# Kernel tuning notes

Measured on AMD Instinct MI355X. Metric: run time of the kernel, lower is better.

## Reference

```python
import jax, jax.numpy as jnp
import numpy as np

B, S, D, H = 2, 2048, 1024, 16
DH = D // H
LEVELS, FACTOR = 3, 2


def setup_inputs() -> dict:
    key = jax.random.key(0)
    ks = jax.random.split(key, 12)
    s = 1.0 / np.sqrt(D)
    n = lambda k, shape, sc: (jax.random.normal(k, shape, jnp.float32) * sc)
    return {
        "query": n(ks[0], (B, S, D), 1.0),
        "key": n(ks[1], (B, S, D), 1.0),
        "value": n(ks[2], (B, S, D), 1.0),
        "Wq": n(ks[3], (D, D), s), "bq": jnp.zeros((D,), jnp.float32),
        "Wk": n(ks[4], (D, D), s), "bk": jnp.zeros((D,), jnp.float32),
        "Wv": n(ks[5], (D, D), s), "bv": jnp.zeros((D,), jnp.float32),
        "Wo": n(ks[6], (D, D), s), "bo": jnp.zeros((D,), jnp.float32),
        "w_levels": jnp.ones((LEVELS,), jnp.float32),
    }


def _downsample(m):
    # mean-pool pairs along sequence: [B, S, D] -> [B, S//FACTOR, D]
    b, s, d = m.shape
    sn = s // FACTOR
    return m[:, : sn * FACTOR, :].reshape(b, sn, FACTOR, d).mean(axis=2)


def _mha(q, k, v, Wq, bq, Wk, bk, Wv, bv, Wo, bo):
    b, sq, d = q.shape
    sk = k.shape[1]
    qh = (q @ Wq + bq).reshape(b, sq, H, DH)
    kh = (k @ Wk + bk).reshape(b, sk, H, DH)
    vh = (v @ Wv + bv).reshape(b, sk, H, DH)
    scores = jnp.einsum("bqhd,bkhd->bhqk", qh, kh) / np.sqrt(DH)
    attn = jax.nn.softmax(scores, axis=-1)
    out = jnp.einsum("bhqk,bkhd->bqhd", attn, vh).reshape(b, sq, d)
    return out @ Wo + bo


def reference(query, key, value, Wq, bq, Wk, bk, Wv, bv, Wo, bo, w_levels):
    keys, vals = [key], [value]
    k_, v_ = key, value
    for _ in range(LEVELS - 1):
        k_ = _downsample(k_)
        v_ = _downsample(v_)
        keys.append(k_)
        vals.append(v_)
    acc = None
    for lvl in range(LEVELS):
        o = _mha(query, keys[lvl], vals[lvl], Wq, bq, Wk, bk, Wv, bv, Wo, bo)
        o = o * w_levels[lvl]
        acc = o if acc is None else acc + o
    return acc / w_levels.sum()
```

## Files before the change

kernel.cpp:

```cpp
#include <hip/hip_runtime.h>


#define B_  2
#define S_  2048
#define D_  1024
#define H_  16
#define DH_ 64
#define THR2 10.0f

typedef short s8v __attribute__((ext_vector_type(8)));
typedef float f4v __attribute__((ext_vector_type(4)));
typedef float f16v __attribute__((ext_vector_type(16)));
typedef unsigned int u32x2 __attribute__((ext_vector_type(2)));
typedef unsigned int u32x4 __attribute__((ext_vector_type(4)));

__device__ __forceinline__ unsigned cvtpk(float lo, float hi){
    unsigned r;
    asm volatile("v_cvt_pk_bf16_f32 %0, %1, %2" : "=v"(r) : "v"(lo), "v"(hi));
    return r;
}
__device__ __forceinline__ unsigned short f2bf1(float v){
    unsigned r;
    asm volatile("v_cvt_pk_bf16_f32 %0, %1, %2" : "=v"(r) : "v"(v), "v"(v));
    return (unsigned short)r;
}
__device__ __forceinline__ float bf2f(unsigned short h){
    union { unsigned u; float f; } v; v.u = ((unsigned)h) << 16;
    return v.f;
}
__device__ __forceinline__ float exp2_(float x){
    float r; asm("v_exp_f32 %0, %1" : "=v"(r) : "v"(x)); return r;
}
__device__ __forceinline__ void pswap(unsigned &dst, unsigned &src){
    asm volatile("v_permlane32_swap_b32 %0, %1" : "+v"(dst), "+v"(src));
}
__device__ __forceinline__ int swz(int row, int kb){
    return row*128 + (((kb) ^ (row & 7) ^ ((row >> 3) & 7)) << 4);
}

__global__ __launch_bounds__(256) void wtrans(
    const float* __restrict__ W0, const float* __restrict__ W1,
    const float* __restrict__ W2, const float* __restrict__ W3,
    unsigned short* __restrict__ T0, unsigned short* __restrict__ T1,
    unsigned short* __restrict__ T2, unsigned short* __restrict__ T3)
{
    __shared__ float tl[32][33];
    const float* W = blockIdx.z==0?W0: blockIdx.z==1?W1: blockIdx.z==2?W2:W3;
    unsigned short* T = blockIdx.z==0?T0: blockIdx.z==1?T1: blockIdx.z==2?T2:T3;
    const int t = threadIdx.x;
    const int bk = blockIdx.x*32, bn = blockIdx.y*32;
    {
        int row = t>>3, c4 = (t&7)*4;
        float4 v = *(const float4*)&W[(size_t)(bk+row)*D_ + bn + c4];
        tl[row][c4+0]=v.x; tl[row][c4+1]=v.y; tl[row][c4+2]=v.z; tl[row][c4+3]=v.w;
    }
    __syncthreads();
    {
        int n = t>>3, k4 = (t&7)*4;
        unsigned a = cvtpk(tl[k4+0][n], tl[k4+1][n]);
        unsigned b = cvtpk(tl[k4+2][n], tl[k4+3][n]);
        u32x2 pk = {a, b};
        *(u32x2*)&T[(size_t)(bn+n)*D_ + bk + k4] = pk;
    }
}

template<int MODE, int AF32>
__global__ __launch_bounds__(256) void gemm_mfma(
    const void* __restrict__ Av, const unsigned short* __restrict__ Btw,
    const float* __restrict__ bias, void* __restrict__ Cv, float scale)
{
    const int N_ = D_, K_ = D_;
    __shared__ __align__(16) char lds[65536];
    const int t = threadIdx.x;
    const int l = t & 63, wv = t>>6, g = l>>4, x = l&15;
    const int wr = wv>>1, wc = wv&1;
    const int br = blockIdx.y*128, bc = blockIdx.x*128;
    const float* Af = (const float*)Av;
    const unsigned short* Ab = (const unsigned short*)Av;

    int rw[4], bl[4];
    #pragma unroll
    for (int p=0;p<4;++p){ int u = t + 256*p; rw[p] = u>>3; bl[p] = u&7; }

    f4v acc[4][4];
    #pragma unroll
    for (int i=0;i<4;++i)
        #pragma unroll
        for (int j=0;j<4;++j) acc[i][j] = (f4v){0.f,0.f,0.f,0.f};

    float4 alo[4], ahi[4]; s8v arg[4]; s8v brg[4];
    #pragma unroll
    for (int p=0;p<4;++p){
        if (AF32){
            const float* ap = Af + (size_t)(br+rw[p])*K_ + bl[p]*8;
            alo[p] = *(const float4*)ap; ahi[p] = *(const float4*)(ap+4);
        } else {
            arg[p] = *(const s8v*)(Ab + (size_t)(br+rw[p])*K_ + bl[p]*8);
        }
        brg[p] = *(const s8v*)(Btw + (size_t)(bc+rw[p])*K_ + bl[p]*8);
    }

    int cur = 0;
    for (int kt=0; kt<K_; kt+=64){
        char* AsB = lds + cur*32768;
        char* BsB = AsB + 16384;
        #pragma unroll
        for (int p=0;p<4;++p){
            if (AF32){
                uint4 pk;
                pk.x = cvtpk(alo[p].x, alo[p].y); pk.y = cvtpk(alo[p].z, alo[p].w);
                pk.z = cvtpk(ahi[p].x, ahi[p].y); pk.w = cvtpk(ahi[p].z, ahi[p].w);
                *(uint4*)(AsB + swz(rw[p], bl[p])) = pk;
            } else {
                *(s8v*)(AsB + swz(rw[p], bl[p])) = arg[p];
            }
            *(s8v*)(BsB + swz(rw[p], bl[p])) = brg[p];
        }
        if (kt + 64 < K_){
            #pragma unroll
            for (int p=0;p<4;++p){
                if (AF32){
                    const float* ap = Af + (size_t)(br+rw[p])*K_ + (kt+64) + bl[p]*8;
                    alo[p] = *(const float4*)ap; ahi[p] = *(const float4*)(ap+4);
                } else {
                    arg[p] = *(const s8v*)(Ab + (size_t)(br+rw[p])*K_ + (kt+64) + bl[p]*8);
                }
                brg[p] = *(const s8v*)(Btw + (size_t)(bc+rw[p])*K_ + (kt+64) + bl[p]*8);
            }
        }
        __syncthreads();
        #pragma unroll
        for (int c=0;c<2;++c){
            s8v af[4], bf[4];
            #pragma unroll
            for (int fm=0; fm<4; ++fm)
                af[fm] = *(const s8v*)(AsB + swz(wr*64+fm*16+x, c*4+g));
            #pragma unroll
            for (int fn=0; fn<4; ++fn)
                bf[fn] = *(const s8v*)(BsB + swz(wc*64+fn*16+x, c*4+g));
            __builtin_amdgcn_s_setprio(1);
            #pragma unroll
            for (int fm=0; fm<4; ++fm)
                #pragma unroll
                for (int fn=0; fn<4; ++fn)
                    acc[fm][fn] = __builtin_amdgcn_mfma_f32_16x16x32_bf16(
                        af[fm], bf[fn], acc[fm][fn], 0,0,0);
            __builtin_amdgcn_s_setprio(0);
        }
        cur ^= 1;
    }

    #pragma unroll
    for (int fn=0; fn<4; ++fn){
        int col = bc + wc*64 + fn*16 + x;
        float bv = bias[col];
        #pragma unroll
        for (int fm=0; fm<4; ++fm){
            int row0 = br + wr*64 + fm*16 + g*4;
            float v0 = (acc[fm][fn][0] + bv);
            float v1 = (acc[fm][fn][1] + bv);
            float v2 = (acc[fm][fn][2] + bv);
            float v3 = (acc[fm][fn][3] + bv);
            if (MODE == 0){
                float* C = (float*)Cv;
                C[(size_t)(row0+0)*N_ + col] = v0;
                C[(size_t)(row0+1)*N_ + col] = v1;
                C[(size_t)(row0+2)*N_ + col] = v2;
                C[(size_t)(row0+3)*N_ + col] = v3;
            } else if (MODE == 1){
                unsigned short* C = (unsigned short*)Cv;
                int hI = col>>6, dhI = col & (DH_-1);
                #pragma unroll
                for (int r=0;r<4;++r){
                    int row = row0 + r;
                    int bI = row>>11, sI = row & (S_-1);
                    float vv = (r==0?v0: r==1?v1: r==2?v2: v3) * scale;
                    C[(((size_t)(bI*H_+hI))*S_+sI)*DH_+dhI] = f2bf1(vv);
                }
            } else {
                unsigned short* C = (unsigned short*)Cv;
                int bI = row0>>11, sI = row0 & (S_-1);
                int hI = col>>6, dhI = col & (DH_-1);
                u32x2 pk;
                pk.x = cvtpk(v0*scale, v1*scale);
                pk.y = cvtpk(v2*scale, v3*scale);
                *(u32x2*)&C[(((size_t)(bI*H_+hI))*DH_+dhI)*S_ + sI] = pk;
            }
        }
    }
}

__global__ __launch_bounds__(256) void pool2_bf16(
    const unsigned short* __restrict__ in, unsigned short* __restrict__ out,
    int nOut4, int Sin)
{
    int idx = blockIdx.x * 256 + threadIdx.x;
    if (idx >= nOut4) return;
    int d0   = (idx & 15) * 4;
    int rest = idx >> 4;
    int Sout = Sin >> 1;
    int so = rest % Sout;
    int bh = rest / Sout;
    size_t base = ((size_t)bh * Sin + 2*so) * DH_ + d0;
    ushort4 a = *(const ushort4*)&in[base];
    ushort4 c = *(const ushort4*)&in[base + DH_];
    ushort4 o;
    o.x = f2bf1(0.5f*(bf2f(a.x)+bf2f(c.x)));
    o.y = f2bf1(0.5f*(bf2f(a.y)+bf2f(c.y)));
    o.z = f2bf1(0.5f*(bf2f(a.z)+bf2f(c.z)));
    o.w = f2bf1(0.5f*(bf2f(a.w)+bf2f(c.w)));
    *(ushort4*)&out[(size_t)idx*4] = o;
}

__global__ __launch_bounds__(256) void pool2T(
    const unsigned short* __restrict__ in, unsigned short* __restrict__ out,
    int nOut4, int Sin, int shift)
{
    int idx = blockIdx.x * 256 + threadIdx.x;
    if (idx >= nOut4) return;
    int row = idx >> shift;
    int so4 = (idx & ((1<<shift)-1)) << 2;
    union { u32x4 u; unsigned short h[8]; } a;
    a.u = *(const u32x4*)&in[(size_t)row*Sin + so4*2];
    float m0 = 0.5f*(bf2f(a.h[0])+bf2f(a.h[1]));
    float m1 = 0.5f*(bf2f(a.h[2])+bf2f(a.h[3]));
    float m2 = 0.5f*(bf2f(a.h[4])+bf2f(a.h[5]));
    float m3 = 0.5f*(bf2f(a.h[6])+bf2f(a.h[7]));
    u32x2 pk; pk.x = cvtpk(m0,m1); pk.y = cvtpk(m2,m3);
    *(u32x2*)&out[(size_t)row*(Sin>>1) + so4] = pk;
}

__global__ __launch_bounds__(256, 2) void attn_mfma5(
    const unsigned short* __restrict__ qh,
    const unsigned short* __restrict__ kh0, const unsigned short* __restrict__ kh1,
    const unsigned short* __restrict__ kh2,
    const unsigned short* __restrict__ vt0, const unsigned short* __restrict__ vt1,
    const unsigned short* __restrict__ vt2,
    const float* __restrict__ wlv, unsigned short* __restrict__ accOut)
{
    __shared__ __align__(16) char ksm[2][8192];
    __shared__ __align__(16) char vsm[2][8192];
    const int t = threadIdx.x, l = t&63, wv = t>>6, q = l&31, hi = l>>5;
    const int bid = blockIdx.x;
    const int qt = bid & 15, h = (bid>>4) & (H_-1), b = bid >> 8;

    const float w0 = wlv[0], w1 = wlv[1], w2 = wlv[2];
    const float winv = 1.f/(w0+w1+w2);

    const unsigned short* qp =
        qh + (((size_t)(b*H_+h))*S_ + (size_t)qt*128 + wv*32 + q)*DH_ + hi*8;
    s8v qf0 = *(const s8v*)(qp);
    s8v qf1 = *(const s8v*)(qp + 16);
    s8v qf2 = *(const s8v*)(qp + 32);
    s8v qf3 = *(const s8v*)(qp + 48);

    const int r0 = t>>3, kb = t&7;
    const int off0 = swz(r0, kb), off1 = swz(r0+32, kb);

    f16v aO0, aO1;
    #pragma unroll
    for (int r=0;r<16;++r){ aO0[r]=0.f; aO1[r]=0.f; }

    int cur = 0;
    #pragma unroll 1
    for (int lvl = 0; lvl < 3; ++lvl) {
        const unsigned short *kp, *vpt; int nt; float wc;
        if (lvl == 0)      { kp = kh0; vpt = vt0; nt = 32; wc = w0; }
        else if (lvl == 1) { kp = kh1; vpt = vt1; nt = 16; wc = w1; }
        else               { kp = kh2; vpt = vt2; nt = 8;  wc = w2; }
        const int Sl = nt*64;
        const unsigned short* kbase = kp + (size_t)(b*H_+h)*Sl*DH_;
        const unsigned short* v0r = vpt + ((size_t)(b*H_+h)*DH_ + r0)*Sl;
        const unsigned short* v1r = vpt + ((size_t)(b*H_+h)*DH_ + r0+32)*Sl;

        float m_i = -1e30f, l_i = 0.f;
        f16v o0, o1;
        #pragma unroll
        for (int r=0;r<16;++r){ o0[r]=0.f; o1[r]=0.f; }

        s8v krg0 = *(const s8v*)(kbase + (size_t)r0*DH_ + kb*8);
        s8v krg1 = *(const s8v*)(kbase + (size_t)(r0+32)*DH_ + kb*8);
        s8v vrg0 = *(const s8v*)(v0r + kb*8);
        s8v vrg1 = *(const s8v*)(v1r + kb*8);

        for (int kt = 0; kt < nt; ++kt) {
            char* kb_ = ksm[cur];
            char* vb_ = vsm[cur];
            *(s8v*)(kb_ + off0) = krg0;
            *(s8v*)(kb_ + off1) = krg1;
            *(s8v*)(vb_ + off0) = vrg0;
            *(s8v*)(vb_ + off1) = vrg1;
            if (kt + 1 < nt) {
                size_t nb = (size_t)(kt+1)*64;
                krg0 = *(const s8v*)(kbase + (nb+r0)*DH_ + kb*8);
                krg1 = *(const s8v*)(kbase + (nb+r0+32)*DH_ + kb*8);
                vrg0 = *(const s8v*)(v0r + nb + kb*8);
                vrg1 = *(const s8v*)(v1r + nb + kb*8);
            }
            __syncthreads();

            f16v s0, s1;
            #pragma unroll
            for (int r=0;r<16;++r){ s0[r]=0.f; s1[r]=0.f; }
            {
                s8v k00 = *(const s8v*)(kb_ + swz(q,      0*2+hi));
                s8v k01 = *(const s8v*)(kb_ + swz(q,      1*2+hi));
                s8v k02 = *(const s8v*)(kb_ + swz(q,      2*2+hi));
                s8v k03 = *(const s8v*)(kb_ + swz(q,      3*2+hi));
                s8v k10 = *(const s8v*)(kb_ + swz(32+q,   0*2+hi));
                s8v k11 = *(const s8v*)(kb_ + swz(32+q,   1*2+hi));
                s8v k12 = *(const s8v*)(kb_ + swz(32+q,   2*2+hi));
                s8v k13 = *(const s8v*)(kb_ + swz(32+q,   3*2+hi));
                __builtin_amdgcn_s_setprio(1);
                s0 = __builtin_amdgcn_mfma_f32_32x32x16_bf16(k00, qf0, s0, 0,0,0);
                s1 = __builtin_amdgcn_mfma_f32_32x32x16_bf16(k10, qf0, s1, 0,0,0);
                s0 = __builtin_amdgcn_mfma_f32_32x32x16_bf16(k01, qf1, s0, 0,0,0);
                s1 = __builtin_amdgcn_mfma_f32_32x32x16_bf16(k11, qf1, s1, 0,0,0);
                s0 = __builtin_amdgcn_mfma_f32_32x32x16_bf16(k02, qf2, s0, 0,0,0);
                s1 = __builtin_amdgcn_mfma_f32_32x32x16_bf16(k12, qf2, s1, 0,0,0);
                s0 = __builtin_amdgcn_mfma_f32_32x32x16_bf16(k03, qf3, s0, 0,0,0);
                s1 = __builtin_amdgcn_mfma_f32_32x32x16_bf16(k13, qf3, s1, 0,0,0);
                __builtin_amdgcn_s_setprio(0);
            }

            float pm = s0[0];
            #pragma unroll
            for (int r=1;r<16;++r) pm = fmaxf(pm, s0[r]);
            #pragma unroll
            for (int r=0;r<16;++r) pm = fmaxf(pm, s1[r]);
            pm = fmaxf(pm, __shfl_xor(pm, 32, 64));
            if (__any(pm > m_i + THR2)) {
                float mn = fmaxf(m_i, pm);
                float corr = exp2_(m_i - mn);
                m_i = mn;
                l_i *= corr;
                #pragma unroll
                for (int r=0;r<16;++r){
                    float cb = __shfl(corr, ((r&3)+8*(r>>2)) + 4*hi, 64);
                    o0[r] *= cb; o1[r] *= cb;
                }
            }
            float rs = 0.f;
            #pragma unroll
            for (int r=0;r<16;++r){ s0[r] = exp2_(s0[r]-m_i); rs += s0[r]; }
            #pragma unroll
            for (int r=0;r<16;++r){ s1[r] = exp2_(s1[r]-m_i); rs += s1[r]; }
            rs += __shfl_xor(rs, 32, 64);
            l_i += rs;

            unsigned a0 = cvtpk(s0[0], s0[1]),  a1 = cvtpk(s0[2], s0[3]);
            unsigned b0 = cvtpk(s0[4], s0[5]),  b1 = cvtpk(s0[6], s0[7]);
            pswap(a0, b0); pswap(a1, b1);
            unsigned c0 = cvtpk(s0[8], s0[9]),  c1 = cvtpk(s0[10], s0[11]);
            unsigned d0 = cvtpk(s0[12], s0[13]),d1 = cvtpk(s0[14], s0[15]);
            pswap(c0, d0); pswap(c1, d1);
            unsigned e0 = cvtpk(s1[0], s1[1]),  e1 = cvtpk(s1[2], s1[3]);
            unsigned f0 = cvtpk(s1[4], s1[5]),  f1 = cvtpk(s1[6], s1[7]);
            pswap(e0, f0); pswap(e1, f1);
            unsigned g0 = cvtpk(s1[8], s1[9]),  g1 = cvtpk(s1[10], s1[11]);
            unsigned h0 = cvtpk(s1[12], s1[13]),h1 = cvtpk(s1[14], s1[15]);
            pswap(g0, h0); pswap(g1, h1);
            union { u32x4 u; s8v s; } pf0, pf1, pf2, pf3;
            pf0.u = (u32x4){a0, a1, b0, b1};
            pf1.u = (u32x4){c0, c1, d0, d1};
            pf2.u = (u32x4){e0, e1, f0, f1};
            pf3.u = (u32x4){g0, g1, h0, h1};

            {
                s8v v00 = *(const s8v*)(vb_ + swz(q,    0*2+hi));
                s8v v01 = *(const s8v*)(vb_ + swz(q,    1*2+hi));
                s8v v02 = *(const s8v*)(vb_ + swz(q,    2*2+hi));
                s8v v03 = *(const s8v*)(vb_ + swz(q,    3*2+hi));
                s8v v10 = *(const s8v*)(vb_ + swz(32+q, 0*2+hi));
                s8v v11 = *(const s8v*)(vb_ + swz(32+q, 1*2+hi));
                s8v v12 = *(const s8v*)(vb_ + swz(32+q, 2*2+hi));
                s8v v13 = *(const s8v*)(vb_ + swz(32+q, 3*2+hi));
                __builtin_amdgcn_s_setprio(1);
                o0 = __builtin_amdgcn_mfma_f32_32x32x16_bf16(pf0.s, v00, o0, 0,0,0);
                o1 = __builtin_amdgcn_mfma_f32_32x32x16_bf16(pf0.s, v10, o1, 0,0,0);
                o0 = __builtin_amdgcn_mfma_f32_32x32x16_bf16(pf1.s, v01, o0, 0,0,0);
                o1 = __builtin_amdgcn_mfma_f32_32x32x16_bf16(pf1.s, v11, o1, 0,0,0);
                o0 = __builtin_amdgcn_mfma_f32_32x32x16_bf16(pf2.s, v02, o0, 0,0,0);
                o1 = __builtin_amdgcn_mfma_f32_32x32x16_bf16(pf2.s, v12, o1, 0,0,0);
                o0 = __builtin_amdgcn_mfma_f32_32x32x16_bf16(pf3.s, v03, o0, 0,0,0);
                o1 = __builtin_amdgcn_mfma_f32_32x32x16_bf16(pf3.s, v13, o1, 0,0,0);
                __builtin_amdgcn_s_setprio(0);
            }
            cur ^= 1;
        }

        float wl = wc * winv;
        #pragma unroll
        for (int r=0;r<16;++r){
            float lb = __shfl(l_i, ((r&3)+8*(r>>2)) + 4*hi, 64);
            float sc = wl / lb;
            aO0[r] += o0[r] * sc;
            aO1[r] += o1[r] * sc;
        }
    }

    #pragma unroll
    for (int r=0;r<16;++r){
        int qrow = ((r&3)+8*(r>>2)) + 4*hi;
        size_t row = (size_t)b*S_ + (size_t)qt*128 + wv*32 + qrow;
        accOut[row*D_ + h*DH_ + q]      = f2bf1(aO0[r]);
        accOut[row*D_ + h*DH_ + 32 + q] = f2bf1(aO1[r]);
    }
}

extern "C" void kernel_launch(void* const* d_in, const int* in_sizes, int n_in,
                              void* d_out, int out_size, void* d_ws, size_t ws_size,
                              hipStream_t stream)
{
    const float* query = (const float*)d_in[0];
    const float* key   = (const float*)d_in[1];
    const float* value = (const float*)d_in[2];
    const float* Wq = (const float*)d_in[3];  const float* bq = (const float*)d_in[4];
    const float* Wk = (const float*)d_in[5];  const float* bk = (const float*)d_in[6];
    const float* Wv = (const float*)d_in[7];  const float* bv = (const float*)d_in[8];
    const float* Wo = (const float*)d_in[9];  const float* bo = (const float*)d_in[10];
    const float* wlv = (const float*)d_in[11];

    char* w = (char*)d_ws;
    unsigned short* qhb  = (unsigned short*)(w);
    unsigned short* khb0 = (unsigned short*)(w + 8388608);
    unsigned short* khb1 = (unsigned short*)(w + 16777216);
    unsigned short* khb2 = (unsigned short*)(w + 20971520);
    unsigned short* vtb0 = (unsigned short*)(w + 23068672);
    unsigned short* vtb1 = (unsigned short*)(w + 31457280);
    unsigned short* vtb2 = (unsigned short*)(w + 35651584);
    unsigned short* accb = (unsigned short*)(w + 37748736);
    unsigned short* Wtq  = (unsigned short*)(w + 46137344);
    unsigned short* Wtk  = (unsigned short*)(w + 48234496);
    unsigned short* Wtv  = (unsigned short*)(w + 50331648);
    unsigned short* Wto  = (unsigned short*)(w + 52428800);

    dim3 bb(256);
    wtrans<<<dim3(32,32,4), bb, 0, stream>>>(Wq, Wk, Wv, Wo, Wtq, Wtk, Wtv, Wto);

    const float scale_q = 0.125f * 1.44269504088896f;
    dim3 gg(D_/128, (B_*S_)/128);
    gemm_mfma<1,1><<<gg, bb, 0, stream>>>(query, Wtq, bq, qhb,  scale_q);
    gemm_mfma<1,1><<<gg, bb, 0, stream>>>(key,   Wtk, bk, khb0, 1.0f);
    gemm_mfma<2,1><<<gg, bb, 0, stream>>>(value, Wtv, bv, vtb0, 1.0f);

    int n1 = B_ * H_ * (S_/2) * DH_ / 4;
    int n2 = B_ * H_ * (S_/4) * DH_ / 4;
    pool2_bf16<<<n1/256, bb, 0, stream>>>(khb0, khb1, n1, S_);
    pool2_bf16<<<n2/256, bb, 0, stream>>>(khb1, khb2, n2, S_/2);
    pool2T<<<n1/256, bb, 0, stream>>>(vtb0, vtb1, n1, S_,   8);
    pool2T<<<n2/256, bb, 0, stream>>>(vtb1, vtb2, n2, S_/2, 7);

    attn_mfma5<<<B_*H_*(S_/128), bb, 0, stream>>>(qhb, khb0, khb1, khb2,
                                                  vtb0, vtb1, vtb2, wlv, accb);

    gemm_mfma<0,0><<<gg, bb, 0, stream>>>(accb, Wto, bo, d_out, 1.0f);
}
```

Measured before the change: 189.5 us.

## Split attention levels across two block groups and sum partials in output GEMM

```diff
diff --git a/kernel.cpp b/kernel.cpp
--- a/kernel.cpp
+++ b/kernel.cpp
@@ -33,6 +33,12 @@
 }
 __device__ __forceinline__ void pswap(unsigned &dst, unsigned &src){
     asm volatile("v_permlane32_swap_b32 %0, %1" : "+v"(dst), "+v"(src));
+}
+__device__ __forceinline__ unsigned addpk(unsigned x, unsigned y){
+    union { unsigned u; float f; } a, b, c, d;
+    a.u = x << 16;          b.u = y << 16;
+    c.u = x & 0xFFFF0000u;  d.u = y & 0xFFFF0000u;
+    return cvtpk(a.f + b.f, c.f + d.f);
 }
 __device__ __forceinline__ int swz(int row, int kb){
     return row*128 + (((kb) ^ (row & 7) ^ ((row >> 3) & 7)) << 4);
@@ -64,10 +70,10 @@
     }
 }
 
-template<int MODE, int AF32>
-__global__ __launch_bounds__(256) void gemm_mfma(
-    const void* __restrict__ Av, const unsigned short* __restrict__ Btw,
-    const float* __restrict__ bias, void* __restrict__ Cv, float scale)
+template<int MODE>
+__global__ __launch_bounds__(256) void gemm_proj(
+    const float* __restrict__ Af, const unsigned short* __restrict__ Btw,
+    const float* __restrict__ bias, unsigned short* __restrict__ C, float scale)
 {
     const int N_ = D_, K_ = D_;
     __shared__ __align__(16) char lds[65536];
@@ -75,8 +81,6 @@
     const int l = t & 63, wv = t>>6, g = l>>4, x = l&15;
     const int wr = wv>>1, wc = wv&1;
     const int br = blockIdx.y*128, bc = blockIdx.x*128;
-    const float* Af = (const float*)Av;
-    const unsigned short* Ab = (const unsigned short*)Av;
 
     int rw[4], bl[4];
     #pragma unroll
@@ -88,15 +92,11 @@
         #pragma unroll
         for (int j=0;j<4;++j) acc[i][j] = (f4v){0.f,0.f,0.f,0.f};
 
-    float4 alo[4], ahi[4]; s8v arg[4]; s8v brg[4];
+    float4 alo[4], ahi[4]; s8v brg[4];
     #pragma unroll
     for (int p=0;p<4;++p){
-        if (AF32){
-            const float* ap = Af + (size_t)(br+rw[p])*K_ + bl[p]*8;
-            alo[p] = *(const float4*)ap; ahi[p] = *(const float4*)(ap+4);
-        } else {
-            arg[p] = *(const s8v*)(Ab + (size_t)(br+rw[p])*K_ + bl[p]*8);
-        }
+        const float* ap = Af + (size_t)(br+rw[p])*K_ + bl[p]*8;
+        alo[p] = *(const float4*)ap; ahi[p] = *(const float4*)(ap+4);
         brg[p] = *(const s8v*)(Btw + (size_t)(bc+rw[p])*K_ + bl[p]*8);
     }
 
@@ -106,25 +106,17 @@
         char* BsB = AsB + 16384;
         #pragma unroll
         for (int p=0;p<4;++p){
-            if (AF32){
-                uint4 pk;
-                pk.x = cvtpk(alo[p].x, alo[p].y); pk.y = cvtpk(alo[p].z, alo[p].w);
-                pk.z = cvtpk(ahi[p].x, ahi[p].y); pk.w = cvtpk(ahi[p].z, ahi[p].w);
-                *(uint4*)(AsB + swz(rw[p], bl[p])) = pk;
-            } else {
-                *(s8v*)(AsB + swz(rw[p], bl[p])) = arg[p];
-            }
+            uint4 pk;
+            pk.x = cvtpk(alo[p].x, alo[p].y); pk.y = cvtpk(alo[p].z, alo[p].w);
+            pk.z = cvtpk(ahi[p].x, ahi[p].y); pk.w = cvtpk(ahi[p].z, ahi[p].w);
+            *(uint4*)(AsB + swz(rw[p], bl[p])) = pk;
             *(s8v*)(BsB + swz(rw[p], bl[p])) = brg[p];
         }
         if (kt + 64 < K_){
             #pragma unroll
             for (int p=0;p<4;++p){
-                if (AF32){
-                    const float* ap = Af + (size_t)(br+rw[p])*K_ + (kt+64) + bl[p]*8;
-                    alo[p] = *(const float4*)ap; ahi[p] = *(const float4*)(ap+4);
-                } else {
-                    arg[p] = *(const s8v*)(Ab + (size_t)(br+rw[p])*K_ + (kt+64) + bl[p]*8);
-                }
+                const float* ap = Af + (size_t)(br+rw[p])*K_ + (kt+64) + bl[p]*8;
+                alo[p] = *(const float4*)ap; ahi[p] = *(const float4*)(ap+4);
                 brg[p] = *(const s8v*)(Btw + (size_t)(bc+rw[p])*K_ + (kt+64) + bl[p]*8);
             }
         }
@@ -157,18 +149,11 @@
         #pragma unroll
         for (int fm=0; fm<4; ++fm){
             int row0 = br + wr*64 + fm*16 + g*4;
-            float v0 = (acc[fm][fn][0] + bv);
-            float v1 = (acc[fm][fn][1] + bv);
-            float v2 = (acc[fm][fn][2] + bv);
-            float v3 = (acc[fm][fn][3] + bv);
-            if (MODE == 0){
-                float* C = (float*)Cv;
-                C[(size_t)(row0+0)*N_ + col] = v0;
-                C[(size_t)(row0+1)*N_ + col] = v1;
-                C[(size_t)(row0+2)*N_ + col] = v2;
-                C[(size_t)(row0+3)*N_ + col] = v3;
-            } else if (MODE == 1){
-                unsigned short* C = (unsigned short*)Cv;
+            float v0 = acc[fm][fn][0] + bv;
+            float v1 = acc[fm][fn][1] + bv;
+            float v2 = acc[fm][fn][2] + bv;
+            float v3 = acc[fm][fn][3] + bv;
+            if (MODE == 1){
                 int hI = col>>6, dhI = col & (DH_-1);
                 #pragma unroll
                 for (int r=0;r<4;++r){
@@ -178,7 +163,6 @@
                     C[(((size_t)(bI*H_+hI))*S_+sI)*DH_+dhI] = f2bf1(vv);
                 }
             } else {
-                unsigned short* C = (unsigned short*)Cv;
                 int bI = row0>>11, sI = row0 & (S_-1);
                 int hI = col>>6, dhI = col & (DH_-1);
                 u32x2 pk;
@@ -190,59 +174,146 @@
     }
 }
 
-__global__ __launch_bounds__(256) void pool2_bf16(
-    const unsigned short* __restrict__ in, unsigned short* __restrict__ out,
-    int nOut4, int Sin)
+__global__ __launch_bounds__(256) void gemm_sum(
+    const unsigned short* __restrict__ A0, const unsigned short* __restrict__ A1,
+    const unsigned short* __restrict__ Btw, const float* __restrict__ bias,
+    float* __restrict__ C)
 {
-    int idx = blockIdx.x * 256 + threadIdx.x;
-    if (idx >= nOut4) return;
-    int d0   = (idx & 15) * 4;
-    int rest = idx >> 4;
-    int Sout = Sin >> 1;
-    int so = rest % Sout;
-    int bh = rest / Sout;
-    size_t base = ((size_t)bh * Sin + 2*so) * DH_ + d0;
-    ushort4 a = *(const ushort4*)&in[base];
-    ushort4 c = *(const ushort4*)&in[base + DH_];
-    ushort4 o;
-    o.x = f2bf1(0.5f*(bf2f(a.x)+bf2f(c.x)));
-    o.y = f2bf1(0.5f*(bf2f(a.y)+bf2f(c.y)));
-    o.z = f2bf1(0.5f*(bf2f(a.z)+bf2f(c.z)));
-    o.w = f2bf1(0.5f*(bf2f(a.w)+bf2f(c.w)));
-    *(ushort4*)&out[(size_t)idx*4] = o;
-}
-
-__global__ __launch_bounds__(256) void pool2T(
-    const unsigned short* __restrict__ in, unsigned short* __restrict__ out,
+    const int N_ = D_, K_ = D_;
+    __shared__ __align__(16) char lds[65536];
+    const int t = threadIdx.x;
+    const int l = t & 63, wv = t>>6, g = l>>4, x = l&15;
+    const int wr = wv>>1, wc = wv&1;
+    const int br = blockIdx.y*128, bc = blockIdx.x*128;
+
+    int rw[4], bl[4];
+    #pragma unroll
+    for (int p=0;p<4;++p){ int u = t + 256*p; rw[p] = u>>3; bl[p] = u&7; }
+
+    f4v acc[4][4];
+    #pragma unroll
+    for (int i=0;i<4;++i)
+        #pragma unroll
+        for (int j=0;j<4;++j) acc[i][j] = (f4v){0.f,0.f,0.f,0.f};
+
+    u32x4 a0r[4], a1r[4]; s8v brg[4];
+    #pragma unroll
+    for (int p=0;p<4;++p){
+        a0r[p] = *(const u32x4*)(A0 + (size_t)(br+rw[p])*K_ + bl[p]*8);
+        a1r[p] = *(const u32x4*)(A1 + (size_t)(br+rw[p])*K_ + bl[p]*8);
+        brg[p] = *(const s8v*)(Btw + (size_t)(bc+rw[p])*K_ + bl[p]*8);
+    }
+
+    int cur = 0;
+    for (int kt=0; kt<K_; kt+=64){
+        char* AsB = lds + cur*32768;
+        char* BsB = AsB + 16384;
+        #pragma unroll
+        for (int p=0;p<4;++p){
+            uint4 pk;
+            pk.x = addpk(a0r[p].x, a1r[p].x);
+            pk.y = addpk(a0r[p].y, a1r[p].y);
+            pk.z = addpk(a0r[p].z, a1r[p].z);
+            pk.w = addpk(a0r[p].w, a1r[p].w);
+            *(uint4*)(AsB + swz(rw[p], bl[p])) = pk;
+            *(s8v*)(BsB + swz(rw[p], bl[p])) = brg[p];
+        }
+        if (kt + 64 < K_){
+            #pragma unroll
+            for (int p=0;p<4;++p){
+                a0r[p] = *(const u32x4*)(A0 + (size_t)(br+rw[p])*K_ + (kt+64) + bl[p]*8);
+                a1r[p] = *(const u32x4*)(A1 + (size_t)(br+rw[p])*K_ + (kt+64) + bl[p]*8);
+                brg[p] = *(const s8v*)(Btw + (size_t)(bc+rw[p])*K_ + (kt+64) + bl[p]*8);
+            }
+        }
+        __syncthreads();
+        #pragma unroll
+        for (int c=0;c<2;++c){
+            s8v af[4], bf[4];
+            #pragma unroll
+            for (int fm=0; fm<4; ++fm)
+                af[fm] = *(const s8v*)(AsB + swz(wr*64+fm*16+x, c*4+g));
+            #pragma unroll
+            for (int fn=0; fn<4; ++fn)
+                bf[fn] = *(const s8v*)(BsB + swz(wc*64+fn*16+x, c*4+g));
+            __builtin_amdgcn_s_setprio(1);
+            #pragma unroll
+            for (int fm=0; fm<4; ++fm)
+                #pragma unroll
+                for (int fn=0; fn<4; ++fn)
+                    acc[fm][fn] = __builtin_amdgcn_mfma_f32_16x16x32_bf16(
+                        af[fm], bf[fn], acc[fm][fn], 0,0,0);
+            __builtin_amdgcn_s_setprio(0);
+        }
+        cur ^= 1;
+    }
+
+    #pragma unroll
+    for (int fn=0; fn<4; ++fn){
+        int col = bc + wc*64 + fn*16 + x;
+        float bv = bias[col];
+        #pragma unroll
+        for (int fm=0; fm<4; ++fm){
+            int row0 = br + wr*64 + fm*16 + g*4;
+            #pragma unroll
+            for (int r=0;r<4;++r)
+                C[(size_t)(row0+r)*N_ + col] = acc[fm][fn][r] + bv;
+        }
+    }
+}
+
+__global__ __launch_bounds__(256) void pool_pair(
+    const unsigned short* __restrict__ kin, unsigned short* __restrict__ kout,
+    const unsigned short* __restrict__ vin, unsigned short* __restrict__ vout,
     int nOut4, int Sin, int shift)
 {
     int idx = blockIdx.x * 256 + threadIdx.x;
     if (idx >= nOut4) return;
-    int row = idx >> shift;
-    int so4 = (idx & ((1<<shift)-1)) << 2;
-    union { u32x4 u; unsigned short h[8]; } a;
-    a.u = *(const u32x4*)&in[(size_t)row*Sin + so4*2];
-    float m0 = 0.5f*(bf2f(a.h[0])+bf2f(a.h[1]));
-    float m1 = 0.5f*(bf2f(a.h[2])+bf2f(a.h[3]));
-    float m2 = 0.5f*(bf2f(a.h[4])+bf2f(a.h[5]));
-    float m3 = 0.5f*(bf2f(a.h[6])+bf2f(a.h[7]));
-    u32x2 pk; pk.x = cvtpk(m0,m1); pk.y = cvtpk(m2,m3);
-    *(u32x2*)&out[(size_t)row*(Sin>>1) + so4] = pk;
-}
-
-__global__ __launch_bounds__(256, 2) void attn_mfma5(
+    if (blockIdx.z == 0){
+        int d0 = (idx & 15) * 4;
+        int rest = idx >> 4;
+        int Sout = Sin >> 1;
+        int so = rest % Sout, bh = rest / Sout;
+        size_t base = ((size_t)bh * Sin + 2*so) * DH_ + d0;
+        ushort4 a = *(const ushort4*)&kin[base];
+        ushort4 c = *(const ushort4*)&kin[base + DH_];
+        ushort4 o;
+        o.x = f2bf1(0.5f*(bf2f(a.x)+bf2f(c.x)));
+        o.y = f2bf1(0.5f*(bf2f(a.y)+bf2f(c.y)));
+        o.z = f2bf1(0.5f*(bf2f(a.z)+bf2f(c.z)));
+        o.w = f2bf1(0.5f*(bf2f(a.w)+bf2f(c.w)));
+        *(ushort4*)&kout[(size_t)idx*4] = o;
+    } else {
+        int row = idx >> shift;
+        int so4 = (idx & ((1<<shift)-1)) << 2;
+        union { u32x4 u; unsigned short hh[8]; } a;
+        a.u = *(const u32x4*)&vin[(size_t)row*Sin + so4*2];
+        float m0 = 0.5f*(bf2f(a.hh[0])+bf2f(a.hh[1]));
+        float m1 = 0.5f*(bf2f(a.hh[2])+bf2f(a.hh[3]));
+        float m2 = 0.5f*(bf2f(a.hh[4])+bf2f(a.hh[5]));
+        float m3 = 0.5f*(bf2f(a.hh[6])+bf2f(a.hh[7]));
+        u32x2 pk; pk.x = cvtpk(m0,m1); pk.y = cvtpk(m2,m3);
+        *(u32x2*)&vout[(size_t)row*(Sin>>1) + so4] = pk;
+    }
+}
+
+__global__ __launch_bounds__(256, 2) void attn_mfma7(
     const unsigned short* __restrict__ qh,
     const unsigned short* __restrict__ kh0, const unsigned short* __restrict__ kh1,
     const unsigned short* __restrict__ kh2,
     const unsigned short* __restrict__ vt0, const unsigned short* __restrict__ vt1,
     const unsigned short* __restrict__ vt2,
-    const float* __restrict__ wlv, unsigned short* __restrict__ accOut)
+    const float* __restrict__ wlv,
+    unsigned short* __restrict__ acc0, unsigned short* __restrict__ acc1)
 {
     __shared__ __align__(16) char ksm[2][8192];
     __shared__ __align__(16) char vsm[2][8192];
     const int t = threadIdx.x, l = t&63, wv = t>>6, q = l&31, hi = l>>5;
     const int bid = blockIdx.x;
     const int qt = bid & 15, h = (bid>>4) & (H_-1), b = bid >> 8;
+    const int grp = blockIdx.y;
+    const int lvB = grp ? 1 : 0, lvE = grp ? 3 : 1;
+    unsigned short* accOut = grp ? acc1 : acc0;
 
     const float w0 = wlv[0], w1 = wlv[1], w2 = wlv[2];
     const float winv = 1.f/(w0+w1+w2);
@@ -263,7 +334,7 @@
 
     int cur = 0;
     #pragma unroll 1
-    for (int lvl = 0; lvl < 3; ++lvl) {
+    for (int lvl = lvB; lvl < lvE; ++lvl) {
         const unsigned short *kp, *vpt; int nt; float wc;
         if (lvl == 0)      { kp = kh0; vpt = vt0; nt = 32; wc = w0; }
         else if (lvl == 1) { kp = kh1; vpt = vt1; nt = 16; wc = w1; }
@@ -429,30 +500,29 @@
     unsigned short* vtb0 = (unsigned short*)(w + 23068672);
     unsigned short* vtb1 = (unsigned short*)(w + 31457280);
     unsigned short* vtb2 = (unsigned short*)(w + 35651584);
-    unsigned short* accb = (unsigned short*)(w + 37748736);
-    unsigned short* Wtq  = (unsigned short*)(w + 46137344);
-    unsigned short* Wtk  = (unsigned short*)(w + 48234496);
-    unsigned short* Wtv  = (unsigned short*)(w + 50331648);
-    unsigned short* Wto  = (unsigned short*)(w + 52428800);
+    unsigned short* acc0 = (unsigned short*)(w + 37748736);
+    unsigned short* Wto  = (unsigned short*)(w + 46137344);
+    unsigned short* Wtq  = (unsigned short*)(w + 48234496);
+    unsigned short* Wtk  = (unsigned short*)(w + 50331648);
+    unsigned short* Wtv  = (unsigned short*)(w + 52428800);
+    unsigned short* acc1 = (unsigned short*)(w + 48234496);
 
     dim3 bb(256);
     wtrans<<<dim3(32,32,4), bb, 0, stream>>>(Wq, Wk, Wv, Wo, Wtq, Wtk, Wtv, Wto);
 
     const float scale_q = 0.125f * 1.44269504088896f;
     dim3 gg(D_/128, (B_*S_)/128);
-    gemm_mfma<1,1><<<gg, bb, 0, stream>>>(query, Wtq, bq, qhb,  scale_q);
-    gemm_mfma<1,1><<<gg, bb, 0, stream>>>(key,   Wtk, bk, khb0, 1.0f);
-    gemm_mfma<2,1><<<gg, bb, 0, stream>>>(value, Wtv, bv, vtb0, 1.0f);
+    gemm_proj<1><<<gg, bb, 0, stream>>>(query, Wtq, bq, qhb,  scale_q);
+    gemm_proj<1><<<gg, bb, 0, stream>>>(key,   Wtk, bk, khb0, 1.0f);
+    gemm_proj<2><<<gg, bb, 0, stream>>>(value, Wtv, bv, vtb0, 1.0f);
 
     int n1 = B_ * H_ * (S_/2) * DH_ / 4;
     int n2 = B_ * H_ * (S_/4) * DH_ / 4;
-    pool2_bf16<<<n1/256, bb, 0, stream>>>(khb0, khb1, n1, S_);
-    pool2_bf16<<<n2/256, bb, 0, stream>>>(khb1, khb2, n2, S_/2);
-    pool2T<<<n1/256, bb, 0, stream>>>(vtb0, vtb1, n1, S_,   8);
-    pool2T<<<n2/256, bb, 0, stream>>>(vtb1, vtb2, n2, S_/2, 7);
-
-    attn_mfma5<<<B_*H_*(S_/128), bb, 0, stream>>>(qhb, khb0, khb1, khb2,
-                                                  vtb0, vtb1, vtb2, wlv, accb);
-
-    gemm_mfma<0,0><<<gg, bb, 0, stream>>>(accb, Wto, bo, d_out, 1.0f);
-}
+    pool_pair<<<dim3(n1/256,1,2), bb, 0, stream>>>(khb0, khb1, vtb0, vtb1, n1, S_,   8);
+    pool_pair<<<dim3(n2/256,1,2), bb, 0, stream>>>(khb1, khb2, vtb1, vtb2, n2, S_/2, 7);
+
+    attn_mfma7<<<dim3(512, 2), bb, 0, stream>>>(qhb, khb0, khb1, khb2,
+                                                vtb0, vtb1, vtb2, wlv, acc0, acc1);
+
+    gemm_sum<<<gg, bb, 0, stream>>>(acc0, acc1, Wto, bo, (float*)d_out);
+}
```

Measured after the change: 194.0 us. 1.02x slower.
